# Kernel optimization log

Hardware: AMD Instinct MI355X
Metric: run time of the kernel (lower is better)

The kernel has to match this reference:

```python
import jax, jax.numpy as jnp
import numpy as np

V_TH = 1.0
V_RESET = 0.0
ALPHA = 4.0  # sigmoid surrogate sharpness used by the Triton backward kernel


@jax.custom_vjp
def spike_fn(over_th):
    # Heaviside forward; sigmoid surrogate gradient in backward.
    return (over_th >= 0).astype(over_th.dtype)


def _spike_fwd(over_th):
    return spike_fn(over_th), over_th


def _spike_bwd(over_th, g):
    sig = jax.nn.sigmoid(ALPHA * over_th)
    return (g * (1.0 - sig) * sig * ALPHA,)


spike_fn.defvjp(_spike_fwd, _spike_bwd)


def setup_inputs() -> dict:
    key = jax.random.key(0)
    k1, _ = jax.random.split(key)
    T, B, D = 32, 128, 8192
    x_seq = jax.random.normal(k1, (T, B, D), dtype=jnp.float32)
    v_init = jnp.zeros((B, D), dtype=jnp.float32)  # module init: v = v_reset = 0.0
    return {"x_seq": x_seq, "v_init": v_init}


def reference(x_seq, v_init):
    # IF neuron, multi-step, hard reset:
    #   h_t   = x_t + v_{t-1}
    #   s_t   = H(h_t - v_th)
    #   v_t   = h_t * (1 - s_t) + v_reset * s_t
    def step(v, x):
        h = x + v
        s = spike_fn(h - V_TH)
        v_next = h * (1.0 - s) + V_RESET * s
        return v_next, s

    _, spike_seq = jax.lax.scan(step, v_init, x_seq)
    return spike_seq
```

## Files before the change

kernel.cpp:

```cpp
#include <hip/hip_runtime.h>


typedef float v2f __attribute__((ext_vector_type(2)));

template <int T, int C>
__global__ __launch_bounds__(256) void if_node_mc_pf2(
    const float* __restrict__ x,
    const float* __restrict__ v0,
    float* __restrict__ out,
    long q)
{
    long i = (long)blockIdx.x * blockDim.x + threadIdx.x;
    if (i >= q) return;

    const v2f* __restrict__ x2 = (const v2f*)x;
    v2f*       __restrict__ o2 = (v2f*)out;
    const v2f* __restrict__ vv = (const v2f*)v0;

    const long n2 = q * C;

    v2f v[C];
#pragma unroll
    for (int c = 0; c < C; ++c)
        v[c] = vv[i + (long)c * q];

    v2f buf[3][C];

#pragma unroll
    for (int c = 0; c < C; ++c)
        buf[0][c] = x2[(long)0 * n2 + i + (long)c * q];
#pragma unroll
    for (int c = 0; c < C; ++c)
        buf[1][c] = x2[(long)1 * n2 + i + (long)c * q];
    __builtin_amdgcn_sched_barrier(0);

#pragma unroll
    for (int t = 0; t < T; ++t) {
        if (t + 2 < T) {
            const int ps = (t + 2) % 3;
#pragma unroll
            for (int c = 0; c < C; ++c)
                buf[ps][c] = x2[(long)(t + 2) * n2 + i + (long)c * q];
        }
        __builtin_amdgcn_sched_barrier(0);

        const int cs = t % 3;
#pragma unroll
        for (int c = 0; c < C; ++c) {
            float hx = buf[cs][c].x + v[c].x;
            float hy = buf[cs][c].y + v[c].y;
            bool sx = (hx - 1.0f) >= 0.0f;
            bool sy = (hy - 1.0f) >= 0.0f;
            v2f s;
            s.x = sx ? 1.0f : 0.0f;
            s.y = sy ? 1.0f : 0.0f;
            v[c].x = sx ? 0.0f : hx;
            v[c].y = sy ? 0.0f : hy;
            __builtin_nontemporal_store(s, &o2[(long)t * n2 + i + (long)c * q]);
        }
        __builtin_amdgcn_sched_barrier(0);
    }
}

__global__ __launch_bounds__(256) void if_node_f2_generic(
    const float* __restrict__ x, const float* __restrict__ v0,
    float* __restrict__ out, long n2, int T)
{
    long i = (long)blockIdx.x * blockDim.x + threadIdx.x;
    if (i >= n2) return;
    const v2f* x2 = (const v2f*)x;
    v2f*       o2 = (v2f*)out;
    v2f v = ((const v2f*)v0)[i];
    for (int t = 0; t < T; ++t) {
        v2f xv = x2[(long)t * n2 + i];
        float hx = xv.x + v.x;
        float hy = xv.y + v.y;
        bool sx = (hx - 1.0f) >= 0.0f;
        bool sy = (hy - 1.0f) >= 0.0f;
        v2f s;
        s.x = sx ? 1.0f : 0.0f;
        s.y = sy ? 1.0f : 0.0f;
        v.x = sx ? 0.0f : hx;
        v.y = sy ? 0.0f : hy;
        o2[(long)t * n2 + i] = s;
    }
}

__global__ __launch_bounds__(256) void if_node_scalar(
    const float* __restrict__ x, const float* __restrict__ v0,
    float* __restrict__ out, long n, int T)
{
    long i = (long)blockIdx.x * blockDim.x + threadIdx.x;
    if (i >= n) return;
    float v = v0[i];
    for (int t = 0; t < T; ++t) {
        float h = x[(long)t * n + i] + v;
        bool s = (h - 1.0f) >= 0.0f;
        out[(long)t * n + i] = s ? 1.0f : 0.0f;
        v = s ? 0.0f : h;
    }
}

extern "C" void kernel_launch(void* const* d_in, const int* in_sizes, int n_in,
                              void* d_out, int out_size, void* d_ws, size_t ws_size,
                              hipStream_t stream) {
    const float* x  = (const float*)d_in[0];
    const float* v0 = (const float*)d_in[1];
    float* out = (float*)d_out;

    long n = in_sizes[1];
    int  T = (int)(in_sizes[0] / n);

    int block = 256;
    constexpr int C = 4;
    if (T == 32 && (n % (2 * C)) == 0) {
        long n2 = n >> 1;
        long q  = n2 / C;
        long grid = (q + block - 1) / block;
        if_node_mc_pf2<32, C><<<dim3((unsigned)grid), dim3(block), 0, stream>>>(
            x, v0, out, q);
    } else if ((n & 1) == 0) {
        long n2 = n >> 1;
        long grid = (n2 + block - 1) / block;
        if_node_f2_generic<<<dim3((unsigned)grid), dim3(block), 0, stream>>>(
            x, v0, out, n2, T);
    } else {
        long grid = (n + block - 1) / block;
        if_node_scalar<<<dim3((unsigned)grid), dim3(block), 0, stream>>>(
            x, v0, out, n, T);
    }
}
```

Before: 231.3 us.

## Split IF kernel into load/compute phase with bit-packed spikes, then store phase

Replaces the 4-chunk float2 kernel with a float4-per-thread kernel. Each thread keeps a 4-deep load prefetch ring, packs all spike results into 32-bit masks in registers, and writes every output in a separate pass after the whole time loop. This separates read and write traffic into distinct phases and widens memory accesses to 16 bytes. In exchange the per-thread memory-level parallelism changes from 4 independent chunks to one, and there is a tail phase that does only stores. The threshold compare is also simplified to h >= 1.

```diff
diff --git a/kernel.cpp b/kernel.cpp
--- a/kernel.cpp
+++ b/kernel.cpp
@@ -1,64 +1,63 @@
 #include <hip/hip_runtime.h>
 
 
+typedef float v4f __attribute__((ext_vector_type(4)));
 typedef float v2f __attribute__((ext_vector_type(2)));
 
-template <int T, int C>
-__global__ __launch_bounds__(256) void if_node_mc_pf2(
+template <int T, int D>
+__global__ __launch_bounds__(256) void if_node_f4_bits(
     const float* __restrict__ x,
     const float* __restrict__ v0,
     float* __restrict__ out,
-    long q)
+    long n4)
 {
     long i = (long)blockIdx.x * blockDim.x + threadIdx.x;
-    if (i >= q) return;
+    if (i >= n4) return;
 
-    const v2f* __restrict__ x2 = (const v2f*)x;
-    v2f*       __restrict__ o2 = (v2f*)out;
-    const v2f* __restrict__ vv = (const v2f*)v0;
+    const v4f* __restrict__ x4 = (const v4f*)x;
+    v4f*       __restrict__ o4 = (v4f*)out;
 
-    const long n2 = q * C;
+    v4f v = ((const v4f*)v0)[i];
 
-    v2f v[C];
-#pragma unroll
-    for (int c = 0; c < C; ++c)
-        v[c] = vv[i + (long)c * q];
-
-    v2f buf[3][C];
+    constexpr int S = D + 1;
+    v4f buf[S];
 
 #pragma unroll
-    for (int c = 0; c < C; ++c)
-        buf[0][c] = x2[(long)0 * n2 + i + (long)c * q];
+    for (int t = 0; t < D; ++t)
+        buf[t % S] = x4[(long)t * n4 + i];
+    __builtin_amdgcn_sched_barrier(0);
+
+    static_assert(T % 8 == 0, "bit-pack assumes T % 8 == 0");
+    unsigned bits[T / 8];
 #pragma unroll
-    for (int c = 0; c < C; ++c)
-        buf[1][c] = x2[(long)1 * n2 + i + (long)c * q];
+    for (int w = 0; w < T / 8; ++w) bits[w] = 0u;
+
+#pragma unroll
+    for (int t = 0; t < T; ++t) {
+        if (t + D < T)
+            buf[(t + D) % S] = x4[(long)(t + D) * n4 + i];
+        __builtin_amdgcn_sched_barrier(0);
+
+        v4f xv = buf[t % S];
+#pragma unroll
+        for (int c = 0; c < 4; ++c) {
+            float h = xv[c] + v[c];
+            bool s = h >= 1.0f;
+            bits[t / 8] |= (s ? 1u : 0u) << ((t % 8) * 4 + c);
+            v[c] = s ? 0.0f : h;
+        }
+        __builtin_amdgcn_sched_barrier(0);
+    }
+
     __builtin_amdgcn_sched_barrier(0);
 
 #pragma unroll
     for (int t = 0; t < T; ++t) {
-        if (t + 2 < T) {
-            const int ps = (t + 2) % 3;
+        v4f s;
 #pragma unroll
-            for (int c = 0; c < C; ++c)
-                buf[ps][c] = x2[(long)(t + 2) * n2 + i + (long)c * q];
-        }
-        __builtin_amdgcn_sched_barrier(0);
-
-        const int cs = t % 3;
-#pragma unroll
-        for (int c = 0; c < C; ++c) {
-            float hx = buf[cs][c].x + v[c].x;
-            float hy = buf[cs][c].y + v[c].y;
-            bool sx = (hx - 1.0f) >= 0.0f;
-            bool sy = (hy - 1.0f) >= 0.0f;
-            v2f s;
-            s.x = sx ? 1.0f : 0.0f;
-            s.y = sy ? 1.0f : 0.0f;
-            v[c].x = sx ? 0.0f : hx;
-            v[c].y = sy ? 0.0f : hy;
-            __builtin_nontemporal_store(s, &o2[(long)t * n2 + i + (long)c * q]);
-        }
-        __builtin_amdgcn_sched_barrier(0);
+        for (int c = 0; c < 4; ++c)
+            s[c] = ((bits[t / 8] >> ((t % 8) * 4 + c)) & 1u) ? 1.0f : 0.0f;
+        __builtin_nontemporal_store(s, &o4[(long)t * n4 + i]);
     }
 }
 
@@ -75,8 +74,8 @@
         v2f xv = x2[(long)t * n2 + i];
         float hx = xv.x + v.x;
         float hy = xv.y + v.y;
-        bool sx = (hx - 1.0f) >= 0.0f;
-        bool sy = (hy - 1.0f) >= 0.0f;
+        bool sx = hx >= 1.0f;
+        bool sy = hy >= 1.0f;
         v2f s;
         s.x = sx ? 1.0f : 0.0f;
         s.y = sy ? 1.0f : 0.0f;
@@ -95,7 +94,7 @@
     float v = v0[i];
     for (int t = 0; t < T; ++t) {
         float h = x[(long)t * n + i] + v;
-        bool s = (h - 1.0f) >= 0.0f;
+        bool s = h >= 1.0f;
         out[(long)t * n + i] = s ? 1.0f : 0.0f;
         v = s ? 0.0f : h;
     }
@@ -112,13 +111,11 @@
     int  T = (int)(in_sizes[0] / n);
 
     int block = 256;
-    constexpr int C = 4;
-    if (T == 32 && (n % (2 * C)) == 0) {
-        long n2 = n >> 1;
-        long q  = n2 / C;
-        long grid = (q + block - 1) / block;
-        if_node_mc_pf2<32, C><<<dim3((unsigned)grid), dim3(block), 0, stream>>>(
-            x, v0, out, q);
+    if (T == 32 && (n % 4) == 0) {
+        long n4 = n >> 2;
+        long grid = (n4 + block - 1) / block;
+        if_node_f4_bits<32, 4><<<dim3((unsigned)grid), dim3(block), 0, stream>>>(
+            x, v0, out, n4);
     } else if ((n & 1) == 0) {
         long n2 = n >> 1;
         long grid = (n2 + block - 1) / block;
```

Measured after the change: 243.3 us. 1.05x slower.
